# Kernel optimization log

Measured on AMD Instinct MI355X. Metric: run time of the kernel, lower is better.

Reference implementation:

```python
import jax, jax.numpy as jnp
import numpy as np

BN_EPS = 1e-5
NORM_EPS = 1e-12  # F.normalize eps


def setup_inputs() -> dict:
    key = jax.random.key(0)
    ks = jax.random.split(key, 4)
    B, C1, H, W = 32, 2048, 32, 32
    D1, D2, NC = 1024, 256, 1000
    x = jax.random.normal(ks[0], (B, C1, H, W), dtype=jnp.float32)
    w1 = jax.random.normal(ks[1], (D1, C1), dtype=jnp.float32) * 0.01  # init_weights normal 0.01
    gamma = jnp.ones((D1,), dtype=jnp.float32)
    beta = jnp.zeros((D1,), dtype=jnp.float32)
    w2 = jax.random.normal(ks[2], (D2, D1), dtype=jnp.float32) * 0.01
    prototypes = jax.random.normal(ks[3], (NC, D2), dtype=jnp.float32)
    return {"x": x, "w1": w1, "gamma": gamma, "beta": beta, "w2": w2, "prototypes": prototypes}


def _l2_normalize(v, axis):
    n = jnp.sqrt(jnp.sum(v * v, axis=axis, keepdims=True))
    return v / jnp.maximum(n, NORM_EPS)


def reference(x, w1, gamma, beta, w2, prototypes):
    # 1x1 conv (no bias) == channel matmul
    h = jnp.einsum('bchw,dc->bdhw', x, w1)  # [B,D1,H,W]
    # BatchNorm2d (training-mode batch stats, affine)
    mean = jnp.mean(h, axis=(0, 2, 3), keepdims=True)
    var = jnp.var(h, axis=(0, 2, 3), keepdims=True)
    h = (h - mean) * jax.lax.rsqrt(var + BN_EPS)
    h = h * gamma[None, :, None, None] + beta[None, :, None, None]
    h = jax.nn.relu(h)
    # final 1x1 conv
    f = jnp.einsum('bchw,dc->bdhw', h, w2)  # [B,D2,H,W]
    B, D, H, W = f.shape
    f = f.reshape(B, D, H * W)  # flatten(2)
    # L2-normalize over channel dim per spatial position, and prototypes per row
    f_norm = _l2_normalize(f, axis=1)           # [B,D,HW]
    p_norm = _l2_normalize(prototypes, axis=1)  # [N,D]
    # einsum('bdc,nd->bnc').sum(-1) == contract d then sum c in one fused einsum
    sim = jnp.einsum('bdc,nd->bn', f_norm, p_norm)  # [B,N]
    return sim
```

## Files before the change

kernel.cpp:

```cpp
#include <hip/hip_runtime.h>

typedef __bf16 bf16;
typedef __bf16 bf16x4 __attribute__((ext_vector_type(4)));
typedef __bf16 bf16x8 __attribute__((ext_vector_type(8)));
typedef float  f32x4  __attribute__((ext_vector_type(4)));

__device__ inline void async_copy16(void* lds, const void* g) {
  __builtin_amdgcn_global_load_lds((const __attribute__((address_space(1))) void*)g,
                                   (__attribute__((address_space(3))) void*)lds,
                                   16, 0, 0);
}

__global__ __launch_bounds__(256)
void f2bf_kernel(const float* __restrict__ in, bf16* __restrict__ out, int n4) {
  int i = blockIdx.x * 256 + threadIdx.x;
  if (i < n4) {
    float4 v = ((const float4*)in)[i];
    bf16x4 o;
    o[0] = (bf16)v.x; o[1] = (bf16)v.y; o[2] = (bf16)v.z; o[3] = (bf16)v.w;
    ((bf16x4*)out)[i] = o;
  }
}

__global__ __launch_bounds__(256)
void transpose_convert(const float* __restrict__ x, bf16* __restrict__ xb) {
  __shared__ float tile[64][65];
  const int tx = threadIdx.x & 15;
  const int ty = threadIdx.x >> 4;
  const int b   = blockIdx.z;
  const int c0  = blockIdx.y * 64;
  const int hw0 = blockIdx.x * 64;
  const float* xp = x + ((size_t)b * 2048 + c0) * 1024 + hw0;
#pragma unroll
  for (int i = 0; i < 4; ++i) {
    const int c = i * 16 + ty;
    const float4 v = *(const float4*)(xp + (size_t)c * 1024 + tx * 4);
    tile[c][tx * 4 + 0] = v.x; tile[c][tx * 4 + 1] = v.y;
    tile[c][tx * 4 + 2] = v.z; tile[c][tx * 4 + 3] = v.w;
  }
  __syncthreads();
  bf16* op = xb + ((size_t)b * 1024 + hw0) * 2048 + c0;
#pragma unroll
  for (int i = 0; i < 4; ++i) {
    const int hw = i * 16 + ty;
    bf16x4 o;
    o[0] = (bf16)tile[tx * 4 + 0][hw];
    o[1] = (bf16)tile[tx * 4 + 1][hw];
    o[2] = (bf16)tile[tx * 4 + 2][hw];
    o[3] = (bf16)tile[tx * 4 + 3][hw];
    *(bf16x4*)(op + (size_t)hw * 2048 + tx * 4) = o;
  }
}

template <bool F32OUT>
__global__ __launch_bounds__(256, 2)
void gemm_bt(const bf16* __restrict__ A, const bf16* __restrict__ Bt,
             bf16* __restrict__ Cb, float* __restrict__ Cf,
             const int K, const int N) {
  __shared__ bf16 As[128 * 64];
  __shared__ bf16 Bs[128 * 64];
  const int tid  = threadIdx.x;
  const int wave = tid >> 6;
  const int lane = tid & 63;
  const int bm = blockIdx.x, bn = blockIdx.y;
  const int wr = wave >> 1, wc = wave & 1;
  const int srow = lane >> 3;
  const int scol = lane & 7;

  f32x4 acc[4][4];
#pragma unroll
  for (int r = 0; r < 4; ++r)
#pragma unroll
    for (int c = 0; c < 4; ++c) acc[r][c] = (f32x4){0.f, 0.f, 0.f, 0.f};

  const bf16* Ag = A + (size_t)(bm * 128) * K;
  const bf16* Bg = Bt + (size_t)(bn * 128) * K;

  const int mrow = lane & 15;
  const int kq = (lane >> 4) * 8;
  const bf16* Asw = As + (wr * 64) * 64;
  const bf16* Bsw = Bs + (wc * 64) * 64;

  for (int k0 = 0; k0 < K; k0 += 64) {
#pragma unroll
    for (int j = 0; j < 4; ++j) {
      const int row = j * 32 + wave * 8;
      async_copy16((void*)(As + row * 64),
                   (const void*)(Ag + (size_t)(row + srow) * K + k0 + scol * 8));
      async_copy16((void*)(Bs + row * 64),
                   (const void*)(Bg + (size_t)(row + srow) * K + k0 + scol * 8));
    }
    __syncthreads();
#pragma unroll
    for (int kk = 0; kk < 2; ++kk) {
      bf16x8 af[4], bfr[4];
#pragma unroll
      for (int r = 0; r < 4; ++r)
        af[r] = *(const bf16x8*)(Asw + (r * 16 + mrow) * 64 + kk * 32 + kq);
#pragma unroll
      for (int c = 0; c < 4; ++c)
        bfr[c] = *(const bf16x8*)(Bsw + (c * 16 + mrow) * 64 + kk * 32 + kq);
#pragma unroll
      for (int r = 0; r < 4; ++r)
#pragma unroll
        for (int c = 0; c < 4; ++c)
          acc[r][c] = __builtin_amdgcn_mfma_f32_16x16x32_bf16(af[r], bfr[c], acc[r][c], 0, 0, 0);
    }
    __syncthreads();
  }

  const int crow = (lane >> 4) * 4;
  const int ccol = lane & 15;
#pragma unroll
  for (int r = 0; r < 4; ++r)
#pragma unroll
    for (int c = 0; c < 4; ++c)
#pragma unroll
      for (int i = 0; i < 4; ++i) {
        const int gm = bm * 128 + wr * 64 + r * 16 + crow + i;
        const int gn = bn * 128 + wc * 64 + c * 16 + ccol;
        if (F32OUT) Cf[(size_t)gm * N + gn] = acc[r][c][i];
        else        Cb[(size_t)gm * N + gn] = (bf16)acc[r][c][i];
      }
}

__global__ __launch_bounds__(256)
void bn_stats(const bf16* __restrict__ hb, float* __restrict__ S1, float* __restrict__ S2) {
  const int c0 = threadIdx.x * 4;
  const int r0 = blockIdx.x * 128;
  float s1[4] = {0, 0, 0, 0}, s2[4] = {0, 0, 0, 0};
  for (int i = 0; i < 128; ++i) {
    const bf16x4 v = *(const bf16x4*)(hb + (size_t)(r0 + i) * 1024 + c0);
#pragma unroll
    for (int j = 0; j < 4; ++j) {
      float xv = (float)v[j];
      s1[j] += xv;
      s2[j] += xv * xv;
    }
  }
#pragma unroll
  for (int j = 0; j < 4; ++j) {
    atomicAdd(&S1[c0 + j], s1[j]);
    atomicAdd(&S2[c0 + j], s2[j]);
  }
}

__global__ void bn_finalize(const float* __restrict__ S1, const float* __restrict__ S2,
                            const float* __restrict__ gamma, const float* __restrict__ beta,
                            float* __restrict__ scale, float* __restrict__ shift) {
  const int d = blockIdx.x * 256 + threadIdx.x;
  const float inv_n = 1.0f / 32768.0f;
  const float mean = S1[d] * inv_n;
  const float var  = S2[d] * inv_n - mean * mean;
  const float rstd = rsqrtf(var + 1e-5f);
  const float sc = gamma[d] * rstd;
  scale[d] = sc;
  shift[d] = beta[d] - mean * sc;
}

__global__ __launch_bounds__(256)
void bn_relu(const bf16* __restrict__ hb, const float* __restrict__ scale,
             const float* __restrict__ shift, bf16* __restrict__ hn) {
  const size_t i = ((size_t)blockIdx.x * 256 + threadIdx.x) * 4;
  const int k = (int)(i & 1023);
  const bf16x4 v = *(const bf16x4*)(hb + i);
  const float4 sc = *(const float4*)(scale + k);
  const float4 sh = *(const float4*)(shift + k);
  bf16x4 o;
  o[0] = (bf16)fmaxf(0.f, (float)v[0] * sc.x + sh.x);
  o[1] = (bf16)fmaxf(0.f, (float)v[1] * sc.y + sh.y);
  o[2] = (bf16)fmaxf(0.f, (float)v[2] * sc.z + sh.z);
  o[3] = (bf16)fmaxf(0.f, (float)v[3] * sc.w + sh.w);
  *(bf16x4*)(hn + i) = o;
}

__global__ __launch_bounds__(256)
void rownorm_g(const float* __restrict__ f, float* __restrict__ g) {
  __shared__ float buf[4][256];
  const int wave = threadIdx.x >> 6, lane = threadIdx.x & 63;
  const int b = blockIdx.x >> 3;
  const int r0 = (blockIdx.x & 7) * 128;
  float a0 = 0, a1 = 0, a2 = 0, a3 = 0;
  for (int i = 0; i < 32; ++i) {
    const int m = b * 1024 + r0 + wave * 32 + i;
    const float4 v = *(const float4*)(f + (size_t)m * 256 + lane * 4);
    float ss = v.x * v.x + v.y * v.y + v.z * v.z + v.w * v.w;
#pragma unroll
    for (int msk = 1; msk < 64; msk <<= 1) ss += __shfl_xor(ss, msk, 64);
    const float inv = 1.0f / fmaxf(sqrtf(ss), 1e-12f);
    a0 += v.x * inv; a1 += v.y * inv; a2 += v.z * inv; a3 += v.w * inv;
  }
  buf[wave][lane * 4 + 0] = a0;
  buf[wave][lane * 4 + 1] = a1;
  buf[wave][lane * 4 + 2] = a2;
  buf[wave][lane * 4 + 3] = a3;
  __syncthreads();
  const int col = threadIdx.x;
  const float s = buf[0][col] + buf[1][col] + buf[2][col] + buf[3][col];
  atomicAdd(&g[b * 256 + col], s);
}

__global__ __launch_bounds__(256)
void sim_kernel(const float* __restrict__ g, const float* __restrict__ protos,
                float* __restrict__ out) {
  const int wave = threadIdx.x >> 6, lane = threadIdx.x & 63;
  const int n = blockIdx.x * 4 + wave;
  const float4 p = *(const float4*)(protos + (size_t)n * 256 + lane * 4);
  float ss = p.x * p.x + p.y * p.y + p.z * p.z + p.w * p.w;
#pragma unroll
  for (int msk = 1; msk < 64; msk <<= 1) ss += __shfl_xor(ss, msk, 64);
  const float inv = 1.0f / fmaxf(sqrtf(ss), 1e-12f);
  const float px = p.x * inv, py = p.y * inv, pz = p.z * inv, pw = p.w * inv;
  for (int b = 0; b < 32; ++b) {
    const float4 gv = *(const float4*)(g + b * 256 + lane * 4);
    float d = px * gv.x + py * gv.y + pz * gv.z + pw * gv.w;
#pragma unroll
    for (int msk = 1; msk < 64; msk <<= 1) d += __shfl_xor(d, msk, 64);
    if (lane == 0) out[b * 1000 + n] = d;
  }
}

extern "C" void kernel_launch(void* const* d_in, const int* in_sizes, int n_in,
                              void* d_out, int out_size, void* d_ws, size_t ws_size,
                              hipStream_t stream) {
  const float* x      = (const float*)d_in[0];
  const float* w1     = (const float*)d_in[1];
  const float* gamma  = (const float*)d_in[2];
  const float* beta   = (const float*)d_in[3];
  const float* w2     = (const float*)d_in[4];
  const float* protos = (const float*)d_in[5];
  float* out = (float*)d_out;

  char* ws = (char*)d_ws;
  bf16*  xb    = (bf16*)(ws);
  bf16*  hn    = (bf16*)(ws);
  float* f     = (float*)(ws + (size_t)67108864);
  bf16*  hb    = (bf16*)(ws + (size_t)134217728);
  bf16*  w1b   = (bf16*)(ws + (size_t)201326592);
  bf16*  w2b   = (bf16*)(ws + (size_t)205520896);
  float* S1    = (float*)(ws + (size_t)206045184);
  float* S2    = (float*)(ws + (size_t)206049280);
  float* scale = (float*)(ws + (size_t)206053376);
  float* shift = (float*)(ws + (size_t)206057472);
  float* g     = (float*)(ws + (size_t)206061568);

  hipMemsetAsync(S1, 0, 8192, stream);
  hipMemsetAsync(g, 0, 32768, stream);

  f2bf_kernel<<<2048, 256, 0, stream>>>(w1, w1b, 524288);
  f2bf_kernel<<<256, 256, 0, stream>>>(w2, w2b, 65536);
  transpose_convert<<<dim3(16, 32, 32), 256, 0, stream>>>(x, xb);
  gemm_bt<false><<<dim3(256, 8), 256, 0, stream>>>(xb, w1b, hb, nullptr, 2048, 1024);
  bn_stats<<<256, 256, 0, stream>>>(hb, S1, S2);
  bn_finalize<<<4, 256, 0, stream>>>(S1, S2, gamma, beta, scale, shift);
  bn_relu<<<32768, 256, 0, stream>>>(hb, scale, shift, hn);
  gemm_bt<true><<<dim3(256, 2), 256, 0, stream>>>(hn, w2b, nullptr, f, 1024, 256);
  rownorm_g<<<256, 256, 0, stream>>>(f, g);
  sim_kernel<<<250, 256, 0, stream>>>(g, protos, out);
}
```

Before: 700.2 us.

## Swizzle GEMM LDS layout, swap grid order, and replace BN atomics with partials

```diff
diff --git a/kernel.cpp b/kernel.cpp
--- a/kernel.cpp
+++ b/kernel.cpp
@@ -53,7 +53,7 @@
 }
 
 template <bool F32OUT>
-__global__ __launch_bounds__(256, 2)
+__global__ __launch_bounds__(256, 4)
 void gemm_bt(const bf16* __restrict__ A, const bf16* __restrict__ Bt,
              bf16* __restrict__ Cb, float* __restrict__ Cf,
              const int K, const int N) {
@@ -62,10 +62,10 @@
   const int tid  = threadIdx.x;
   const int wave = tid >> 6;
   const int lane = tid & 63;
-  const int bm = blockIdx.x, bn = blockIdx.y;
+  const int bm = blockIdx.y, bn = blockIdx.x;
   const int wr = wave >> 1, wc = wave & 1;
   const int srow = lane >> 3;
-  const int scol = lane & 7;
+  const int scol = (lane & 7) ^ srow;
 
   f32x4 acc[4][4];
 #pragma unroll
@@ -77,7 +77,8 @@
   const bf16* Bg = Bt + (size_t)(bn * 128) * K;
 
   const int mrow = lane & 15;
-  const int kq = (lane >> 4) * 8;
+  const int kq = lane >> 4;
+  const int sw = mrow & 7;
   const bf16* Asw = As + (wr * 64) * 64;
   const bf16* Bsw = Bs + (wc * 64) * 64;
 
@@ -94,12 +95,13 @@
 #pragma unroll
     for (int kk = 0; kk < 2; ++kk) {
       bf16x8 af[4], bfr[4];
+      const int lc = kk * 4 + kq;
 #pragma unroll
       for (int r = 0; r < 4; ++r)
-        af[r] = *(const bf16x8*)(Asw + (r * 16 + mrow) * 64 + kk * 32 + kq);
+        af[r] = *(const bf16x8*)(Asw + (r * 16 + mrow) * 64 + ((lc ^ sw) * 8));
 #pragma unroll
       for (int c = 0; c < 4; ++c)
-        bfr[c] = *(const bf16x8*)(Bsw + (c * 16 + mrow) * 64 + kk * 32 + kq);
+        bfr[c] = *(const bf16x8*)(Bsw + (c * 16 + mrow) * 64 + ((lc ^ sw) * 8));
 #pragma unroll
       for (int r = 0; r < 4; ++r)
 #pragma unroll
@@ -125,33 +127,49 @@
 }
 
 __global__ __launch_bounds__(256)
-void bn_stats(const bf16* __restrict__ hb, float* __restrict__ S1, float* __restrict__ S2) {
-  const int c0 = threadIdx.x * 4;
-  const int r0 = blockIdx.x * 128;
-  float s1[4] = {0, 0, 0, 0}, s2[4] = {0, 0, 0, 0};
-  for (int i = 0; i < 128; ++i) {
-    const bf16x4 v = *(const bf16x4*)(hb + (size_t)(r0 + i) * 1024 + c0);
-#pragma unroll
-    for (int j = 0; j < 4; ++j) {
-      float xv = (float)v[j];
-      s1[j] += xv;
-      s2[j] += xv * xv;
+void bn_stats(const bf16* __restrict__ hb, float* __restrict__ P) {
+  __shared__ float ls1[2][128][9];
+  __shared__ float ls2[2][128][9];
+  const int t = threadIdx.x;
+  const int c = t & 127, rg = t >> 7;
+  const bf16* hp = hb + (size_t)blockIdx.x * 128 * 1024 + c * 8;
+  float s1[8], s2[8];
+#pragma unroll
+  for (int j = 0; j < 8; ++j) { s1[j] = 0.f; s2[j] = 0.f; }
+  for (int i = 0; i < 64; ++i) {
+    const bf16x8 v = *(const bf16x8*)(hp + (size_t)(i * 2 + rg) * 1024);
+#pragma unroll
+    for (int j = 0; j < 8; ++j) {
+      const float xv = (float)v[j];
+      s1[j] += xv; s2[j] += xv * xv;
     }
   }
 #pragma unroll
-  for (int j = 0; j < 4; ++j) {
-    atomicAdd(&S1[c0 + j], s1[j]);
-    atomicAdd(&S2[c0 + j], s2[j]);
-  }
-}
-
-__global__ void bn_finalize(const float* __restrict__ S1, const float* __restrict__ S2,
-                            const float* __restrict__ gamma, const float* __restrict__ beta,
-                            float* __restrict__ scale, float* __restrict__ shift) {
+  for (int j = 0; j < 8; ++j) { ls1[rg][c][j] = s1[j]; ls2[rg][c][j] = s2[j]; }
+  __syncthreads();
+  float* Pb = P + (size_t)blockIdx.x * 2048;
+  if (rg == 0) {
+#pragma unroll
+    for (int j = 0; j < 8; ++j) Pb[c * 8 + j] = ls1[0][c][j] + ls1[1][c][j];
+  } else {
+#pragma unroll
+    for (int j = 0; j < 8; ++j) Pb[1024 + c * 8 + j] = ls2[0][c][j] + ls2[1][c][j];
+  }
+}
+
+__global__ __launch_bounds__(256)
+void bn_finalize(const float* __restrict__ P,
+                 const float* __restrict__ gamma, const float* __restrict__ beta,
+                 float* __restrict__ scale, float* __restrict__ shift) {
   const int d = blockIdx.x * 256 + threadIdx.x;
+  float s1 = 0.f, s2 = 0.f;
+  for (int p = 0; p < 256; ++p) {
+    s1 += P[(size_t)p * 2048 + d];
+    s2 += P[(size_t)p * 2048 + 1024 + d];
+  }
   const float inv_n = 1.0f / 32768.0f;
-  const float mean = S1[d] * inv_n;
-  const float var  = S2[d] * inv_n - mean * mean;
+  const float mean = s1 * inv_n;
+  const float var  = s2 * inv_n - mean * mean;
   const float rstd = rsqrtf(var + 1e-5f);
   const float sc = gamma[d] * rstd;
   scale[d] = sc;
@@ -161,17 +179,20 @@
 __global__ __launch_bounds__(256)
 void bn_relu(const bf16* __restrict__ hb, const float* __restrict__ scale,
              const float* __restrict__ shift, bf16* __restrict__ hn) {
-  const size_t i = ((size_t)blockIdx.x * 256 + threadIdx.x) * 4;
+  const size_t i = ((size_t)blockIdx.x * 256 + threadIdx.x) * 8;
   const int k = (int)(i & 1023);
-  const bf16x4 v = *(const bf16x4*)(hb + i);
-  const float4 sc = *(const float4*)(scale + k);
-  const float4 sh = *(const float4*)(shift + k);
-  bf16x4 o;
-  o[0] = (bf16)fmaxf(0.f, (float)v[0] * sc.x + sh.x);
-  o[1] = (bf16)fmaxf(0.f, (float)v[1] * sc.y + sh.y);
-  o[2] = (bf16)fmaxf(0.f, (float)v[2] * sc.z + sh.z);
-  o[3] = (bf16)fmaxf(0.f, (float)v[3] * sc.w + sh.w);
-  *(bf16x4*)(hn + i) = o;
+  const bf16x8 v = *(const bf16x8*)(hb + i);
+  bf16x8 o;
+#pragma unroll
+  for (int j = 0; j < 8; j += 4) {
+    const float4 sc = *(const float4*)(scale + k + j);
+    const float4 sh = *(const float4*)(shift + k + j);
+    o[j + 0] = (bf16)fmaxf(0.f, (float)v[j + 0] * sc.x + sh.x);
+    o[j + 1] = (bf16)fmaxf(0.f, (float)v[j + 1] * sc.y + sh.y);
+    o[j + 2] = (bf16)fmaxf(0.f, (float)v[j + 2] * sc.z + sh.z);
+    o[j + 3] = (bf16)fmaxf(0.f, (float)v[j + 3] * sc.w + sh.w);
+  }
+  *(bf16x8*)(hn + i) = o;
 }
 
 __global__ __launch_bounds__(256)
@@ -235,26 +256,24 @@
   bf16*  xb    = (bf16*)(ws);
   bf16*  hn    = (bf16*)(ws);
   float* f     = (float*)(ws + (size_t)67108864);
+  float* P     = (float*)(ws + (size_t)100663296);
   bf16*  hb    = (bf16*)(ws + (size_t)134217728);
   bf16*  w1b   = (bf16*)(ws + (size_t)201326592);
   bf16*  w2b   = (bf16*)(ws + (size_t)205520896);
-  float* S1    = (float*)(ws + (size_t)206045184);
-  float* S2    = (float*)(ws + (size_t)206049280);
-  float* scale = (float*)(ws + (size_t)206053376);
-  float* shift = (float*)(ws + (size_t)206057472);
-  float* g     = (float*)(ws + (size_t)206061568);
-
-  hipMemsetAsync(S1, 0, 8192, stream);
+  float* scale = (float*)(ws + (size_t)206045184);
+  float* shift = (float*)(ws + (size_t)206049280);
+  float* g     = (float*)(ws + (size_t)206053376);
+
   hipMemsetAsync(g, 0, 32768, stream);
 
   f2bf_kernel<<<2048, 256, 0, stream>>>(w1, w1b, 524288);
   f2bf_kernel<<<256, 256, 0, stream>>>(w2, w2b, 65536);
   transpose_convert<<<dim3(16, 32, 32), 256, 0, stream>>>(x, xb);
-  gemm_bt<false><<<dim3(256, 8), 256, 0, stream>>>(xb, w1b, hb, nullptr, 2048, 1024);
-  bn_stats<<<256, 256, 0, stream>>>(hb, S1, S2);
-  bn_finalize<<<4, 256, 0, stream>>>(S1, S2, gamma, beta, scale, shift);
-  bn_relu<<<32768, 256, 0, stream>>>(hb, scale, shift, hn);
-  gemm_bt<true><<<dim3(256, 2), 256, 0, stream>>>(hn, w2b, nullptr, f, 1024, 256);
+  gemm_bt<false><<<dim3(8, 256), 256, 0, stream>>>(xb, w1b, hb, nullptr, 2048, 1024);
+  bn_stats<<<256, 256, 0, stream>>>(hb, P);
+  bn_finalize<<<4, 256, 0, stream>>>(P, gamma, beta, scale, shift);
+  bn_relu<<<16384, 256, 0, stream>>>(hb, scale, shift, hn);
+  gemm_bt<true><<<dim3(2, 256), 256, 0, stream>>>(hn, w2b, nullptr, f, 1024, 256);
   rownorm_g<<<256, 256, 0, stream>>>(f, g);
   sim_kernel<<<250, 256, 0, stream>>>(g, protos, out);
 }
```

Result: faster. 662.5 us (-5.4%).

## Fuse BN stats into GEMM1 and BN-ReLU plus row-normalize into GEMM2

Applied to the files above, without the earlier changes.

```diff
diff --git a/kernel.cpp b/kernel.cpp
--- a/kernel.cpp
+++ b/kernel.cpp
@@ -52,20 +52,21 @@
   }
 }
 
-template <bool F32OUT>
-__global__ __launch_bounds__(256, 2)
-void gemm_bt(const bf16* __restrict__ A, const bf16* __restrict__ Bt,
-             bf16* __restrict__ Cb, float* __restrict__ Cf,
-             const int K, const int N) {
-  __shared__ bf16 As[128 * 64];
-  __shared__ bf16 Bs[128 * 64];
+__global__ __launch_bounds__(256, 4)
+void gemm1(const bf16* __restrict__ A, const bf16* __restrict__ Bt,
+           bf16* __restrict__ Cb, float* __restrict__ S1, float* __restrict__ S2) {
+  __shared__ __align__(16) bf16 As[128 * 64];
+  __shared__ __align__(16) bf16 Bs[128 * 64];
+  const int K = 2048, N = 1024;
   const int tid  = threadIdx.x;
   const int wave = tid >> 6;
   const int lane = tid & 63;
-  const int bm = blockIdx.x, bn = blockIdx.y;
+  const int id = blockIdx.x;
+  const int bm = (id & 7) * 32 + ((id >> 3) >> 3);
+  const int bn = (id >> 3) & 7;
   const int wr = wave >> 1, wc = wave & 1;
   const int srow = lane >> 3;
-  const int scol = lane & 7;
+  const int scol = (lane & 7) ^ srow;
 
   f32x4 acc[4][4];
 #pragma unroll
@@ -77,7 +78,8 @@
   const bf16* Bg = Bt + (size_t)(bn * 128) * K;
 
   const int mrow = lane & 15;
-  const int kq = (lane >> 4) * 8;
+  const int kq = lane >> 4;
+  const int sw = mrow & 7;
   const bf16* Asw = As + (wr * 64) * 64;
   const bf16* Bsw = Bs + (wc * 64) * 64;
 
@@ -94,12 +96,13 @@
 #pragma unroll
     for (int kk = 0; kk < 2; ++kk) {
       bf16x8 af[4], bfr[4];
+      const int lc = kk * 4 + kq;
 #pragma unroll
       for (int r = 0; r < 4; ++r)
-        af[r] = *(const bf16x8*)(Asw + (r * 16 + mrow) * 64 + kk * 32 + kq);
+        af[r] = *(const bf16x8*)(Asw + (r * 16 + mrow) * 64 + ((lc ^ sw) * 8));
 #pragma unroll
       for (int c = 0; c < 4; ++c)
-        bfr[c] = *(const bf16x8*)(Bsw + (c * 16 + mrow) * 64 + kk * 32 + kq);
+        bfr[c] = *(const bf16x8*)(Bsw + (c * 16 + mrow) * 64 + ((lc ^ sw) * 8));
 #pragma unroll
       for (int r = 0; r < 4; ++r)
 #pragma unroll
@@ -119,35 +122,41 @@
       for (int i = 0; i < 4; ++i) {
         const int gm = bm * 128 + wr * 64 + r * 16 + crow + i;
         const int gn = bn * 128 + wc * 64 + c * 16 + ccol;
-        if (F32OUT) Cf[(size_t)gm * N + gn] = acc[r][c][i];
-        else        Cb[(size_t)gm * N + gn] = (bf16)acc[r][c][i];
+        Cb[(size_t)gm * N + gn] = (bf16)acc[r][c][i];
       }
+
+  float s1[4], s2[4];
+#pragma unroll
+  for (int c = 0; c < 4; ++c) {
+    float a = 0.f, b = 0.f;
+#pragma unroll
+    for (int r = 0; r < 4; ++r)
+#pragma unroll
+      for (int i = 0; i < 4; ++i) { const float v = acc[r][c][i]; a += v; b += v * v; }
+#pragma unroll
+    for (int msk = 16; msk < 64; msk <<= 1) { a += __shfl_xor(a, msk, 64); b += __shfl_xor(b, msk, 64); }
+    s1[c] = a; s2[c] = b;
+  }
+  float* S1s = (float*)As;
+  float* S2s = S1s + 256;
+  if ((lane & 15) == lane) {
+#pragma unroll
+    for (int c = 0; c < 4; ++c) {
+      S1s[wr * 128 + wc * 64 + c * 16 + lane] = s1[c];
+      S2s[wr * 128 + wc * 64 + c * 16 + lane] = s2[c];
+    }
+  }
+  __syncthreads();
+  if (tid < 128) {
+    atomicAdd(&S1[bn * 128 + tid], S1s[tid] + S1s[128 + tid]);
+    atomicAdd(&S2[bn * 128 + tid], S2s[tid] + S2s[128 + tid]);
+  }
 }
 
 __global__ __launch_bounds__(256)
-void bn_stats(const bf16* __restrict__ hb, float* __restrict__ S1, float* __restrict__ S2) {
-  const int c0 = threadIdx.x * 4;
-  const int r0 = blockIdx.x * 128;
-  float s1[4] = {0, 0, 0, 0}, s2[4] = {0, 0, 0, 0};
-  for (int i = 0; i < 128; ++i) {
-    const bf16x4 v = *(const bf16x4*)(hb + (size_t)(r0 + i) * 1024 + c0);
-#pragma unroll
-    for (int j = 0; j < 4; ++j) {
-      float xv = (float)v[j];
-      s1[j] += xv;
-      s2[j] += xv * xv;
-    }
-  }
-#pragma unroll
-  for (int j = 0; j < 4; ++j) {
-    atomicAdd(&S1[c0 + j], s1[j]);
-    atomicAdd(&S2[c0 + j], s2[j]);
-  }
-}
-
-__global__ void bn_finalize(const float* __restrict__ S1, const float* __restrict__ S2,
-                            const float* __restrict__ gamma, const float* __restrict__ beta,
-                            float* __restrict__ scale, float* __restrict__ shift) {
+void bn_finalize(const float* __restrict__ S1, const float* __restrict__ S2,
+                 const float* __restrict__ gamma, const float* __restrict__ beta,
+                 float* __restrict__ scale, float* __restrict__ shift) {
   const int d = blockIdx.x * 256 + threadIdx.x;
   const float inv_n = 1.0f / 32768.0f;
   const float mean = S1[d] * inv_n;
@@ -158,46 +167,121 @@
   shift[d] = beta[d] - mean * sc;
 }
 
-__global__ __launch_bounds__(256)
-void bn_relu(const bf16* __restrict__ hb, const float* __restrict__ scale,
-             const float* __restrict__ shift, bf16* __restrict__ hn) {
-  const size_t i = ((size_t)blockIdx.x * 256 + threadIdx.x) * 4;
-  const int k = (int)(i & 1023);
-  const bf16x4 v = *(const bf16x4*)(hb + i);
-  const float4 sc = *(const float4*)(scale + k);
-  const float4 sh = *(const float4*)(shift + k);
-  bf16x4 o;
-  o[0] = (bf16)fmaxf(0.f, (float)v[0] * sc.x + sh.x);
-  o[1] = (bf16)fmaxf(0.f, (float)v[1] * sc.y + sh.y);
-  o[2] = (bf16)fmaxf(0.f, (float)v[2] * sc.z + sh.z);
-  o[3] = (bf16)fmaxf(0.f, (float)v[3] * sc.w + sh.w);
-  *(bf16x4*)(hn + i) = o;
-}
-
-__global__ __launch_bounds__(256)
-void rownorm_g(const float* __restrict__ f, float* __restrict__ g) {
-  __shared__ float buf[4][256];
-  const int wave = threadIdx.x >> 6, lane = threadIdx.x & 63;
-  const int b = blockIdx.x >> 3;
-  const int r0 = (blockIdx.x & 7) * 128;
-  float a0 = 0, a1 = 0, a2 = 0, a3 = 0;
-  for (int i = 0; i < 32; ++i) {
-    const int m = b * 1024 + r0 + wave * 32 + i;
-    const float4 v = *(const float4*)(f + (size_t)m * 256 + lane * 4);
-    float ss = v.x * v.x + v.y * v.y + v.z * v.z + v.w * v.w;
-#pragma unroll
-    for (int msk = 1; msk < 64; msk <<= 1) ss += __shfl_xor(ss, msk, 64);
-    const float inv = 1.0f / fmaxf(sqrtf(ss), 1e-12f);
-    a0 += v.x * inv; a1 += v.y * inv; a2 += v.z * inv; a3 += v.w * inv;
-  }
-  buf[wave][lane * 4 + 0] = a0;
-  buf[wave][lane * 4 + 1] = a1;
-  buf[wave][lane * 4 + 2] = a2;
-  buf[wave][lane * 4 + 3] = a3;
+__global__ __launch_bounds__(512, 4)
+void gemm2f(const bf16* __restrict__ A, const bf16* __restrict__ Bt,
+            const float* __restrict__ scale, const float* __restrict__ shift,
+            float* __restrict__ g) {
+  __shared__ __align__(16) bf16 As[128 * 64];
+  __shared__ __align__(16) bf16 Bs[256 * 64];
+  const int K = 1024;
+  const int tid  = threadIdx.x;
+  const int wave = tid >> 6;
+  const int lane = tid & 63;
+  const int bm = blockIdx.x;
+  const int wr = wave >> 2, wc = wave & 3;
+  const int srow = lane >> 3;
+  const int scol = (lane & 7) ^ srow;
+
+  f32x4 acc[4][4];
+#pragma unroll
+  for (int r = 0; r < 4; ++r)
+#pragma unroll
+    for (int c = 0; c < 4; ++c) acc[r][c] = (f32x4){0.f, 0.f, 0.f, 0.f};
+
+  const bf16* Ag = A + (size_t)(bm * 128) * K;
+
+  const int mrow = lane & 15;
+  const int kq = lane >> 4;
+  const int sw = mrow & 7;
+  const bf16* Asw = As + (wr * 64) * 64;
+  const bf16* Bsw = Bs + (wc * 64) * 64;
+
+  for (int k0 = 0; k0 < K; k0 += 64) {
+#pragma unroll
+    for (int j = 0; j < 2; ++j) {
+      const int row = wave * 16 + j * 8;
+      async_copy16((void*)(As + row * 64),
+                   (const void*)(Ag + (size_t)(row + srow) * K + k0 + scol * 8));
+    }
+#pragma unroll
+    for (int j = 0; j < 4; ++j) {
+      const int row = wave * 32 + j * 8;
+      async_copy16((void*)(Bs + row * 64),
+                   (const void*)(Bt + (size_t)(row + srow) * K + k0 + scol * 8));
+    }
+    __syncthreads();
+#pragma unroll
+    for (int kk = 0; kk < 2; ++kk) {
+      const int lc = kk * 4 + kq;
+      const int kbase = k0 + lc * 8;
+      const float4 sc0 = *(const float4*)(scale + kbase);
+      const float4 sc1 = *(const float4*)(scale + kbase + 4);
+      const float4 sh0 = *(const float4*)(shift + kbase);
+      const float4 sh1 = *(const float4*)(shift + kbase + 4);
+      const float scv[8] = {sc0.x, sc0.y, sc0.z, sc0.w, sc1.x, sc1.y, sc1.z, sc1.w};
+      const float shv[8] = {sh0.x, sh0.y, sh0.z, sh0.w, sh1.x, sh1.y, sh1.z, sh1.w};
+      bf16x8 af[4], bfr[4];
+#pragma unroll
+      for (int r = 0; r < 4; ++r) {
+        bf16x8 a = *(const bf16x8*)(Asw + (r * 16 + mrow) * 64 + ((lc ^ sw) * 8));
+#pragma unroll
+        for (int j = 0; j < 8; ++j)
+          a[j] = (bf16)fmaxf(0.f, fmaf((float)a[j], scv[j], shv[j]));
+        af[r] = a;
+      }
+#pragma unroll
+      for (int c = 0; c < 4; ++c)
+        bfr[c] = *(const bf16x8*)(Bsw + (c * 16 + mrow) * 64 + ((lc ^ sw) * 8));
+#pragma unroll
+      for (int r = 0; r < 4; ++r)
+#pragma unroll
+        for (int c = 0; c < 4; ++c)
+          acc[r][c] = __builtin_amdgcn_mfma_f32_16x16x32_bf16(af[r], bfr[c], acc[r][c], 0, 0, 0);
+    }
+    __syncthreads();
+  }
+
+  float* ss4   = (float*)As;
+  float* inv_s = ss4 + 512;
+  const int q = lane >> 4;
+#pragma unroll
+  for (int r = 0; r < 4; ++r) {
+    float ssv[4];
+#pragma unroll
+    for (int i = 0; i < 4; ++i) {
+      float s = 0.f;
+#pragma unroll
+      for (int c = 0; c < 4; ++c) { const float v = acc[r][c][i]; s += v * v; }
+#pragma unroll
+      for (int msk = 1; msk < 16; msk <<= 1) s += __shfl_xor(s, msk, 64);
+      ssv[i] = s;
+    }
+    if ((lane & 15) == 0)
+#pragma unroll
+      for (int i = 0; i < 4; ++i)
+        ss4[wc * 128 + wr * 64 + r * 16 + q * 4 + i] = ssv[i];
+  }
   __syncthreads();
-  const int col = threadIdx.x;
-  const float s = buf[0][col] + buf[1][col] + buf[2][col] + buf[3][col];
-  atomicAdd(&g[b * 256 + col], s);
+  if (tid < 128) {
+    const float rs = ss4[tid] + ss4[128 + tid] + ss4[256 + tid] + ss4[384 + tid];
+    inv_s[tid] = 1.0f / fmaxf(sqrtf(rs), 1e-12f);
+  }
+  __syncthreads();
+  const int b = bm >> 3;
+  const int ccol = lane & 15;
+#pragma unroll
+  for (int c = 0; c < 4; ++c) {
+    float gl = 0.f;
+#pragma unroll
+    for (int r = 0; r < 4; ++r)
+#pragma unroll
+      for (int i = 0; i < 4; ++i)
+        gl += acc[r][c][i] * inv_s[wr * 64 + r * 16 + q * 4 + i];
+#pragma unroll
+    for (int msk = 16; msk < 64; msk <<= 1) gl += __shfl_xor(gl, msk, 64);
+    if ((lane & 48) == 0)
+      atomicAdd(&g[b * 256 + wc * 64 + c * 16 + ccol], gl);
+  }
 }
 
 __global__ __launch_bounds__(256)
@@ -233,28 +317,22 @@
 
   char* ws = (char*)d_ws;
   bf16*  xb    = (bf16*)(ws);
-  bf16*  hn    = (bf16*)(ws);
-  float* f     = (float*)(ws + (size_t)67108864);
   bf16*  hb    = (bf16*)(ws + (size_t)134217728);
   bf16*  w1b   = (bf16*)(ws + (size_t)201326592);
   bf16*  w2b   = (bf16*)(ws + (size_t)205520896);
   float* S1    = (float*)(ws + (size_t)206045184);
   float* S2    = (float*)(ws + (size_t)206049280);
-  float* scale = (float*)(ws + (size_t)206053376);
-  float* shift = (float*)(ws + (size_t)206057472);
-  float* g     = (float*)(ws + (size_t)206061568);
-
-  hipMemsetAsync(S1, 0, 8192, stream);
-  hipMemsetAsync(g, 0, 32768, stream);
+  float* g     = (float*)(ws + (size_t)206053376);
+  float* scale = (float*)(ws + (size_t)206086144);
+  float* shift = (float*)(ws + (size_t)206090240);
+
+  hipMemsetAsync(S1, 0, 40960, stream);
 
   f2bf_kernel<<<2048, 256, 0, stream>>>(w1, w1b, 524288);
   f2bf_kernel<<<256, 256, 0, stream>>>(w2, w2b, 65536);
   transpose_convert<<<dim3(16, 32, 32), 256, 0, stream>>>(x, xb);
-  gemm_bt<false><<<dim3(256, 8), 256, 0, stream>>>(xb, w1b, hb, nullptr, 2048, 1024);
-  bn_stats<<<256, 256, 0, stream>>>(hb, S1, S2);
+  gemm1<<<2048, 256, 0, stream>>>(xb, w1b, hb, S1, S2);
   bn_finalize<<<4, 256, 0, stream>>>(S1, S2, gamma, beta, scale, shift);
-  bn_relu<<<32768, 256, 0, stream>>>(hb, scale, shift, hn);
-  gemm_bt<true><<<dim3(256, 2), 256, 0, stream>>>(hn, w2b, nullptr, f, 1024, 256);
-  rownorm_g<<<256, 256, 0, stream>>>(f, g);
+  gemm2f<<<256, 512, 0, stream>>>(hb, w2b, scale, shift, g);
   sim_kernel<<<250, 256, 0, stream>>>(g, protos, out);
 }
```

Result: faster. 612.2 us (-12.6%).
